# Performance work log

Measured on AMD Instinct MI355X. Metric: run time of the kernel, lower is better.

## Reference

```python
import jax, jax.numpy as jnp
import numpy as np

K = 6                      # max_displacement / pad_size
WIN = 2 * K + 1            # displacement window side
D = WIN * WIN              # number of affinity channels (169)


def setup_inputs() -> dict:
    key = jax.random.key(0)
    k1, k2 = jax.random.split(key)
    aff = jax.random.normal(k1, (4, D, 192, 192), dtype=jnp.float32)
    input2 = jax.random.normal(k2, (4, 64, 192, 192), dtype=jnp.float32)
    return {"aff": aff, "input2": input2}


def reference(aff, input2):
    # output[b,c,y,x] = sum_{dy,dx in [-k,k]} aff[b, idx(dy,dx), y, x]
    #                   * input2_zeropad[b, c, y+dy, x+dx]
    # Scanned over the (2k+1)^2 displacements to avoid materializing the
    # [B, D, C, H, W] cost-volume intermediate.
    B, C, H, W = input2.shape
    Dn = aff.shape[1]
    win = int(round(Dn ** 0.5))
    k = (win - 1) // 2
    padded = jnp.pad(input2, ((0, 0), (0, 0), (k, k), (k, k)))  # [B,C,H+2k,W+2k]
    aff_t = jnp.transpose(aff, (1, 0, 2, 3))  # [D,B,H,W]
    ds = jnp.arange(Dn)

    def body(acc, xs):
        d, a = xs                      # a: [B,H,W]
        dy = d // win                  # 0..2k (offset into padded rows)
        dx = d % win                   # 0..2k (offset into padded cols)
        patch = jax.lax.dynamic_slice(padded, (0, 0, dy, dx), (B, C, H, W))
        return acc + a[:, None, :, :] * patch, None

    out, _ = jax.lax.scan(body, jnp.zeros_like(input2), (ds, aff_t))
    return out
```

## Files before the change

### kernel.cpp

```cpp
#include <hip/hip_runtime.h>


#define KD   6
#define WIN  13
#define ND   169
#define NB   4
#define NC   64
#define NH   192
#define NW   192
#define XH   64
#define PITCHW 42
#define BUFW (NC * PITCHW)
#define AFFW 832
#define NTH  256

typedef _Float16 half2v __attribute__((ext_vector_type(2)));

static __device__ __forceinline__ half2v h2(unsigned u) {
    return __builtin_bit_cast(half2v, u);
}
static __device__ __forceinline__ unsigned pk(float a, float b) {
    return __builtin_bit_cast(unsigned, __builtin_amdgcn_cvt_pkrtz(a, b));
}
static __device__ __forceinline__ float hget(unsigned w, int sel) {
    const half2v h = h2(w);
    return sel ? (float)h.y : (float)h.x;
}
typedef const __attribute__((address_space(1))) void* gas_t;
typedef __attribute__((address_space(3))) void* sas_t;
static __device__ __forceinline__ void gll16(const float* g, unsigned* l) {
    __builtin_amdgcn_global_load_lds((gas_t)g, (sas_t)l, 16, 0, 0);
}

__global__ __launch_bounds__(NTH)
__attribute__((amdgpu_waves_per_eu(3, 4)))
void mxassemble(const float* __restrict__ aff,
                const float* __restrict__ in2,
                float* __restrict__ out) {
    __shared__ unsigned ldsw[2 * BUFW];
    __shared__ unsigned affw[2 * AFFW];

    const int bx = blockIdx.x;
    const int g  = bx & 7;
    const int k  = bx >> 3;
    const int b  = k / 24;
    const int yl = k - 24 * b;
    const int y  = 24 * g + yl;
    const int xb = blockIdx.y;
    const int X0 = xb * XH;

    const int t    = threadIdx.x;
    const int l    = t & 63;
    const int wv   = t >> 6;
    const int cg   = l & 15;
    const int xs   = l >> 4;
    const int slot = wv * 4 + xs;
    const int x0   = X0 + slot * 4;

    if (xb != 1) {
        const int w0 = (xb == 0) ? 0 : 36;
        if (t < NC * 2) {
            const int c = t >> 1, qq = t & 1;
            *(uint2*)&ldsw[c * PITCHW + w0 + 2 * qq]        = make_uint2(0u, 0u);
            *(uint2*)&ldsw[BUFW + c * PITCHW + w0 + 2 * qq] = make_uint2(0u, 0u);
        }
    }

    int wadr[5], goff[5];
#pragma unroll
    for (int s = 0; s < 5; ++s) {
        const int ii = t + NTH * s;
        const int c  = ii / 20;
        const int q  = ii - 20 * c;
        const int xg = X0 - 8 + 4 * q;
        const bool ok = (xg >= 0) && (xg < NW);
        wadr[s] = ok ? (c * PITCHW + 2 * q) : -1;
        goff[s] = c * (NH * NW) + xg;
    }

    float acc[4][4];
#pragma unroll
    for (int i = 0; i < 4; ++i)
#pragma unroll
        for (int j = 0; j < 4; ++j) acc[i][j] = 0.f;

    const float* in2_b = in2 + (size_t)b * NC * NH * NW;
    const int wbase = cg * PITCHW + 2 * slot;

    const int dxl = t >> 4;
    const int xo4 = (t & 15) * 4;
    const float* gaff = aff + ((size_t)b * ND + dxl) * (NH * NW)
                            + (size_t)y * NW + X0 + xo4;
    unsigned* const affdst = affw + ((t >> 6) << 8);

    if (t < WIN * 16) gll16(gaff, affdst);
    gaff += (size_t)WIN * (NH * NW);
    {
        const int r0 = y - KD;
        if (r0 >= 0) {
            const float* p = in2_b + (size_t)r0 * NW;
            float4 Sv[5];
#pragma unroll
            for (int s = 0; s < 5; ++s)
                if (wadr[s] >= 0) Sv[s] = *(const float4*)&p[goff[s]];
#pragma unroll
            for (int s = 0; s < 5; ++s)
                if (wadr[s] >= 0) {
                    uint2 w; w.x = pk(Sv[s].x, Sv[s].y); w.y = pk(Sv[s].z, Sv[s].w);
                    *(uint2*)&ldsw[wadr[s]] = w;
                }
        }
    }
    __syncthreads();

    for (int rr = 0; rr < WIN; ++rr) {
        const unsigned* cur = ldsw + ((rr & 1) ? BUFW : 0);
        unsigned*       nxt = ldsw + ((rr & 1) ? 0 : BUFW);
        const unsigned* acur = affw + ((rr & 1) ? AFFW : 0) + slot * 4;
        const int  r  = y - KD + rr;
        const bool pv = (r >= 0) && (r < NH);
        const int  rn = r + 1;
        const bool sv = (rr < WIN - 1) && (rn >= 0) && (rn < NH);

        if (rr < WIN - 1) {
            if (t < WIN * 16)
                gll16(gaff, affdst + ((rr & 1) ? 0 : AFFW));
            gaff += (size_t)WIN * (NH * NW);
        }
        float4 Sv[5];
        if (sv) {
            const float* p = in2_b + (size_t)rn * NW;
#pragma unroll
            for (int s = 0; s < 5; ++s)
                if (wadr[s] >= 0) Sv[s] = *(const float4*)&p[goff[s]];
#pragma unroll
            for (int s = 0; s < 5; ++s)
                asm volatile("" : "+v"(Sv[s].x), "+v"(Sv[s].y),
                                  "+v"(Sv[s].z), "+v"(Sv[s].w));
        }
        __builtin_amdgcn_sched_barrier(0);

        if (pv) {
            unsigned W[4][10];
#pragma unroll
            for (int i = 0; i < 4; ++i) {
                const unsigned* wp = cur + wbase + i * (16 * PITCHW);
                *(uint2*)&W[i][0] = *(const uint2*)&wp[0];
                *(uint2*)&W[i][2] = *(const uint2*)&wp[2];
                *(uint2*)&W[i][4] = *(const uint2*)&wp[4];
                *(uint2*)&W[i][6] = *(const uint2*)&wp[6];
                *(uint2*)&W[i][8] = *(const uint2*)&wp[8];
            }
#pragma unroll
            for (int m = 0; m < 3; ++m) {
                alignas(16) float A[4][4];
                *(float4*)&A[0][0] = *(const float4*)&acur[(4*m+0)*64];
                *(float4*)&A[1][0] = *(const float4*)&acur[(4*m+1)*64];
                *(float4*)&A[2][0] = *(const float4*)&acur[(4*m+2)*64];
                *(float4*)&A[3][0] = *(const float4*)&acur[(4*m+3)*64];
#pragma unroll
                for (int i = 0; i < 4; ++i) {
#pragma unroll
                    for (int j = 0; j < 4; ++j) {
                        float a = acc[i][j];
                        a = fmaf(A[0][j], hget(W[i][(j+4*m+2)>>1], (j+4*m+2)&1), a);
                        a = fmaf(A[1][j], hget(W[i][(j+4*m+3)>>1], (j+4*m+3)&1), a);
                        a = fmaf(A[2][j], hget(W[i][(j+4*m+4)>>1], (j+4*m+4)&1), a);
                        a = fmaf(A[3][j], hget(W[i][(j+4*m+5)>>1], (j+4*m+5)&1), a);
                        acc[i][j] = a;
                    }
                }
            }
            {
                alignas(16) float At[4];
                *(float4*)&At[0] = *(const float4*)&acur[12 * 64];
#pragma unroll
                for (int i = 0; i < 4; ++i)
#pragma unroll
                    for (int j = 0; j < 4; ++j)
                        acc[i][j] = fmaf(At[j],
                            hget(W[i][(j+14)>>1], (j+14)&1), acc[i][j]);
            }
        }

        if (sv) {
#pragma unroll
            for (int s = 0; s < 5; ++s)
                if (wadr[s] >= 0) {
                    uint2 w; w.x = pk(Sv[s].x, Sv[s].y); w.y = pk(Sv[s].z, Sv[s].w);
                    *(uint2*)&nxt[wadr[s]] = w;
                }
        }

        __syncthreads();
    }

    float* ob = out + (((size_t)b * NC + cg) * NH + y) * NW + x0;
#pragma unroll
    for (int i = 0; i < 4; ++i) {
        *(float4*)&ob[(size_t)(16 * i) * NH * NW] =
            make_float4(acc[i][0], acc[i][1], acc[i][2], acc[i][3]);
    }
}

extern "C" void kernel_launch(void* const* d_in, const int* in_sizes, int n_in,
                              void* d_out, int out_size, void* d_ws, size_t ws_size,
                              hipStream_t stream) {
    const float* aff = (const float*)d_in[0];
    const float* in2 = (const float*)d_in[1];
    float* outp = (float*)d_out;
    dim3 grid(NB * NH, 3, 1);
    dim3 block(NTH);
    hipLaunchKernelGGL(mxassemble, grid, block, 0, stream, aff, in2, outp);
}
```

Baseline: 281.1 us.

## Pack affinity pairs to fp16 and use fdot2 for displacement accumulation

```diff
diff --git a/kernel.cpp b/kernel.cpp
--- a/kernel.cpp
+++ b/kernel.cpp
@@ -8,10 +8,11 @@
 #define NC   64
 #define NH   192
 #define NW   192
+#define HW   (NH * NW)
 #define XH   64
 #define PITCHW 42
 #define BUFW (NC * PITCHW)
-#define AFFW 832
+#define AFFPW 448
 #define NTH  256
 
 typedef _Float16 half2v __attribute__((ext_vector_type(2)));
@@ -22,23 +23,23 @@
 static __device__ __forceinline__ unsigned pk(float a, float b) {
     return __builtin_bit_cast(unsigned, __builtin_amdgcn_cvt_pkrtz(a, b));
 }
-static __device__ __forceinline__ float hget(unsigned w, int sel) {
-    const half2v h = h2(w);
-    return sel ? (float)h.y : (float)h.x;
-}
-typedef const __attribute__((address_space(1))) void* gas_t;
-typedef __attribute__((address_space(3))) void* sas_t;
-static __device__ __forceinline__ void gll16(const float* g, unsigned* l) {
-    __builtin_amdgcn_global_load_lds((gas_t)g, (sas_t)l, 16, 0, 0);
-}
+
+#if __has_builtin(__builtin_amdgcn_fdot2)
+#define FDOT2(a, b, c) __builtin_amdgcn_fdot2((a), (b), (c), false)
+#else
+static __device__ __forceinline__ float fdot2_fb(half2v a, half2v b, float c) {
+    return fmaf((float)a.x, (float)b.x, fmaf((float)a.y, (float)b.y, c));
+}
+#define FDOT2(a, b, c) fdot2_fb((a), (b), (c))
+#endif
 
 __global__ __launch_bounds__(NTH)
-__attribute__((amdgpu_waves_per_eu(3, 4)))
+__attribute__((amdgpu_waves_per_eu(4, 8)))
 void mxassemble(const float* __restrict__ aff,
                 const float* __restrict__ in2,
                 float* __restrict__ out) {
     __shared__ unsigned ldsw[2 * BUFW];
-    __shared__ unsigned affw[2 * AFFW];
+    __shared__ unsigned apkw[2 * AFFPW];
 
     const int bx = blockIdx.x;
     const int g  = bx & 7;
@@ -75,8 +76,15 @@
         const int xg = X0 - 8 + 4 * q;
         const bool ok = (xg >= 0) && (xg < NW);
         wadr[s] = ok ? (c * PITCHW + 2 * q) : -1;
-        goff[s] = c * (NH * NW) + xg;
-    }
+        goff[s] = c * HW + xg;
+    }
+
+    const int am  = t >> 4;
+    const int axc = t & 15;
+    const bool astg = (t < 112);
+    const float* pA0 = aff + (size_t)b * ND * HW + (size_t)y * NW + X0
+                           + 4 * axc + (size_t)(2 * am) * HW;
+    const int aw = am * 64 + 4 * axc;
 
     float acc[4][4];
 #pragma unroll
@@ -84,17 +92,18 @@
 #pragma unroll
         for (int j = 0; j < 4; ++j) acc[i][j] = 0.f;
 
-    const float* in2_b = in2 + (size_t)b * NC * NH * NW;
+    const float* in2_b = in2 + (size_t)b * NC * HW;
     const int wbase = cg * PITCHW + 2 * slot;
 
-    const int dxl = t >> 4;
-    const int xo4 = (t & 15) * 4;
-    const float* gaff = aff + ((size_t)b * ND + dxl) * (NH * NW)
-                            + (size_t)y * NW + X0 + xo4;
-    unsigned* const affdst = affw + ((t >> 6) << 8);
-
-    if (t < WIN * 16) gll16(gaff, affdst);
-    gaff += (size_t)WIN * (NH * NW);
+    if (astg) {
+        const float4 A0 = *(const float4*)pA0;
+        float4 A1 = make_float4(0.f, 0.f, 0.f, 0.f);
+        if (am < 6) A1 = *(const float4*)(pA0 + HW);
+        uint4 w;
+        w.x = pk(A0.x, A1.x); w.y = pk(A0.y, A1.y);
+        w.z = pk(A0.z, A1.z); w.w = pk(A0.w, A1.w);
+        *(uint4*)&apkw[aw] = w;
+    }
     {
         const int r0 = y - KD;
         if (r0 >= 0) {
@@ -114,18 +123,24 @@
     __syncthreads();
 
     for (int rr = 0; rr < WIN; ++rr) {
-        const unsigned* cur = ldsw + ((rr & 1) ? BUFW : 0);
-        unsigned*       nxt = ldsw + ((rr & 1) ? 0 : BUFW);
-        const unsigned* acur = affw + ((rr & 1) ? AFFW : 0) + slot * 4;
+        const unsigned* cur  = ldsw + ((rr & 1) ? BUFW : 0);
+        unsigned*       nxt  = ldsw + ((rr & 1) ? 0 : BUFW);
+        const unsigned* acur = apkw + ((rr & 1) ? AFFPW : 0) + 4 * slot;
+        unsigned*       anxt = apkw + ((rr & 1) ? 0 : AFFPW);
         const int  r  = y - KD + rr;
         const bool pv = (r >= 0) && (r < NH);
         const int  rn = r + 1;
         const bool sv = (rr < WIN - 1) && (rn >= 0) && (rn < NH);
 
-        if (rr < WIN - 1) {
-            if (t < WIN * 16)
-                gll16(gaff, affdst + ((rr & 1) ? 0 : AFFW));
-            gaff += (size_t)WIN * (NH * NW);
+        float4 A0, A1;
+        const bool av = astg && (rr < WIN - 1);
+        if (av) {
+            const float* p = pA0 + (size_t)((rr + 1) * WIN) * HW;
+            A0 = *(const float4*)p;
+            A1 = make_float4(0.f, 0.f, 0.f, 0.f);
+            if (am < 6) A1 = *(const float4*)(p + HW);
+            asm volatile("" : "+v"(A0.x), "+v"(A0.y), "+v"(A0.z), "+v"(A0.w));
+            asm volatile("" : "+v"(A1.x), "+v"(A1.y), "+v"(A1.z), "+v"(A1.w));
         }
         float4 Sv[5];
         if (sv) {
@@ -152,37 +167,30 @@
                 *(uint2*)&W[i][8] = *(const uint2*)&wp[8];
             }
 #pragma unroll
-            for (int m = 0; m < 3; ++m) {
-                alignas(16) float A[4][4];
-                *(float4*)&A[0][0] = *(const float4*)&acur[(4*m+0)*64];
-                *(float4*)&A[1][0] = *(const float4*)&acur[(4*m+1)*64];
-                *(float4*)&A[2][0] = *(const float4*)&acur[(4*m+2)*64];
-                *(float4*)&A[3][0] = *(const float4*)&acur[(4*m+3)*64];
+            for (int m = 0; m < 7; ++m) {
+                unsigned A4[4];
+                *(uint4*)&A4[0] = *(const uint4*)&acur[m * 64];
 #pragma unroll
                 for (int i = 0; i < 4; ++i) {
-#pragma unroll
-                    for (int j = 0; j < 4; ++j) {
-                        float a = acc[i][j];
-                        a = fmaf(A[0][j], hget(W[i][(j+4*m+2)>>1], (j+4*m+2)&1), a);
-                        a = fmaf(A[1][j], hget(W[i][(j+4*m+3)>>1], (j+4*m+3)&1), a);
-                        a = fmaf(A[2][j], hget(W[i][(j+4*m+4)>>1], (j+4*m+4)&1), a);
-                        a = fmaf(A[3][j], hget(W[i][(j+4*m+5)>>1], (j+4*m+5)&1), a);
-                        acc[i][j] = a;
-                    }
+                    const unsigned p1 = W[i][m + 1];
+                    const unsigned p2 = W[i][m + 2];
+                    const unsigned p3 = W[i][m + 3];
+                    const unsigned s1 = (p1 >> 16) | (p2 << 16);
+                    const unsigned s2 = (p2 >> 16) | (p3 << 16);
+                    acc[i][0] = FDOT2(h2(A4[0]), h2(p1), acc[i][0]);
+                    acc[i][1] = FDOT2(h2(A4[1]), h2(s1), acc[i][1]);
+                    acc[i][2] = FDOT2(h2(A4[2]), h2(p2), acc[i][2]);
+                    acc[i][3] = FDOT2(h2(A4[3]), h2(s2), acc[i][3]);
                 }
             }
-            {
-                alignas(16) float At[4];
-                *(float4*)&At[0] = *(const float4*)&acur[12 * 64];
-#pragma unroll
-                for (int i = 0; i < 4; ++i)
-#pragma unroll
-                    for (int j = 0; j < 4; ++j)
-                        acc[i][j] = fmaf(At[j],
-                            hget(W[i][(j+14)>>1], (j+14)&1), acc[i][j]);
-            }
-        }
-
+        }
+
+        if (av) {
+            uint4 w;
+            w.x = pk(A0.x, A1.x); w.y = pk(A0.y, A1.y);
+            w.z = pk(A0.z, A1.z); w.w = pk(A0.w, A1.w);
+            *(uint4*)&anxt[aw] = w;
+        }
         if (sv) {
 #pragma unroll
             for (int s = 0; s < 5; ++s)
@@ -198,7 +206,7 @@
     float* ob = out + (((size_t)b * NC + cg) * NH + y) * NW + x0;
 #pragma unroll
     for (int i = 0; i < 4; ++i) {
-        *(float4*)&ob[(size_t)(16 * i) * NH * NW] =
+        *(float4*)&ob[(size_t)(16 * i) * HW] =
             make_float4(acc[i][0], acc[i][1], acc[i][2], acc[i][3]);
     }
 }
```

Result: faster. 260.6 us (-7.3%).
